# Performance work log

Hardware: AMD Instinct MI355X
Metric: run time of the kernel (lower is better)

Reference implementation:

```python
import jax, jax.numpy as jnp
import numpy as np

B, S, D = 2, 2048, 1024
H, KVH, HD = 16, 1, 64
E, K, HID = 8, 2, 4096
EPS = 1e-5


def rmsnorm(x, scale):
    ms = jnp.mean(x * x, axis=-1, keepdims=True)
    return x * jax.lax.rsqrt(ms + EPS) * scale


def setup_inputs() -> dict:
    key = jax.random.key(0)
    ks = jax.random.split(key, 12)
    s = lambda k, shape, fan: jax.random.normal(k, shape, jnp.float32) * (fan ** -0.5)
    return {
        "x": jax.random.normal(ks[0], (B, S, D), jnp.float32),
        "g_pre_mqa": jnp.ones((D,), jnp.float32),
        "g_post_mqa": jnp.ones((D,), jnp.float32),
        "g_pre_moe": jnp.ones((D,), jnp.float32),
        "g_post_moe": jnp.ones((D,), jnp.float32),
        "Wq": s(ks[1], (D, H * HD), D),
        "Wk": s(ks[2], (D, KVH * HD), D),
        "Wv": s(ks[3], (D, KVH * HD), D),
        "Wo": s(ks[4], (H * HD, D), H * HD),
        "Wg": s(ks[5], (D, E), D),
        "We1": s(ks[6], (E, D, HID), D),
        "We2": s(ks[7], (E, HID, D), HID),
    }


def mqa(x, Wq, Wk, Wv, Wo):
    b, s, _ = x.shape
    q = (x @ Wq).reshape(b, s, H, HD).transpose(0, 2, 1, 3)     # [B,H,S,hd]
    k = (x @ Wk).reshape(b, s, KVH, HD).transpose(0, 2, 1, 3)   # [B,1,S,hd]
    v = (x @ Wv).reshape(b, s, KVH, HD).transpose(0, 2, 1, 3)
    scores = jnp.einsum('bhqd,bhkd->bhqk', q, jnp.broadcast_to(k, (b, H, s, HD))) / np.sqrt(HD)
    probs = jax.nn.softmax(scores, axis=-1)  # note: no causal mask, matching _standard_attention
    out = jnp.einsum('bhqk,bhkd->bhqd', probs, jnp.broadcast_to(v, (b, H, s, HD)))
    out = out.transpose(0, 2, 1, 3).reshape(b, s, H * HD)
    return out @ Wo


def moe(h, Wg, We1, We2):
    logits = h @ Wg                       # [B,S,E]
    probs = jax.nn.softmax(logits, axis=-1)
    topv, topi = jax.lax.top_k(probs, K)  # [B,S,K]
    # scatter top-k probs into full expert vector (non-chosen experts -> 0)
    routing = jnp.sum(jax.nn.one_hot(topi, E, dtype=h.dtype) * topv[..., None], axis=-2)  # [B,S,E]
    mid = jax.nn.gelu(jnp.einsum('bsd,edh->bseh', h, We1))
    eo = jnp.einsum('bseh,ehd->bsed', mid, We2)
    out = jnp.einsum('bse,bsed->bsd', routing, eo)
    return out, probs


def reference(x, g_pre_mqa, g_post_mqa, g_pre_moe, g_post_moe, Wq, Wk, Wv, Wo, Wg, We1, We2):
    # inference path: dropout and router noise disabled (training=False)
    x = x + rmsnorm(mqa(rmsnorm(x, g_pre_mqa), Wq, Wk, Wv, Wo), g_post_mqa)
    moe_out, routing_probs = moe(rmsnorm(x, g_pre_moe), Wg, We1, We2)
    x = x + rmsnorm(moe_out, g_post_moe)
    return x, routing_probs
```

## Files before the change

kernel.cpp:

```cpp
#include <hip/hip_runtime.h>
#include <hip/hip_bf16.h>
#include <math.h>

#define NTOK   4096
#define DMODEL 1024
#define SEQL   2048
#define QKVW   1152
#define NH     16
#define HDIM   64
#define NE     8
#define HIDD   4096
#define EPSV   1e-5f
#define KT     32

#define ASCL   256.f
#define WSCL   4096.f
#define OUTSCL (1.f/1048576.f)
#define SSCALE (0.125f/65536.f)

typedef __attribute__((ext_vector_type(8))) short bf16x8;
typedef __attribute__((ext_vector_type(8))) _Float16 f16x8;
typedef __attribute__((ext_vector_type(4))) _Float16 f16x4;
typedef __attribute__((ext_vector_type(4))) float f32x4;

#define GLOBAL_AS __attribute__((address_space(1)))
#define LDS_AS    __attribute__((address_space(3)))
__device__ __forceinline__ void gl_lds16(const void* g, void* l){
  __builtin_amdgcn_global_load_lds((const GLOBAL_AS void*)g, (LDS_AS void*)l, 16u, 0, 0u);
}

__device__ __forceinline__ short f2b(float x){
  __hip_bfloat16 h = __float2bfloat16(x);
  return *reinterpret_cast<short*>(&h);
}
__device__ __forceinline__ float b2f(short s){
  __hip_bfloat16 h = *reinterpret_cast<__hip_bfloat16*>(&s);
  return __bfloat162float(h);
}
__device__ __forceinline__ void split3(float x, short& a, short& b, short& c){
  a = f2b(x);
  float r1 = x - b2f(a);
  b = f2b(r1);
  float r2 = r1 - b2f(b);
  c = f2b(r2);
}
__device__ __forceinline__ void split2h(float x, _Float16& a, _Float16& b){
  a = (_Float16)x;
  b = (_Float16)(x - (float)a);
}

__global__ __launch_bounds__(256) void transpose_conv_kernel(
    const float* __restrict__ in, short* __restrict__ out,
    int R, int C, long inb, long outb)
{
  __shared__ float tile[32][33];
  in  += (size_t)blockIdx.z * inb;
  out += (size_t)blockIdx.z * outb;
  int c0 = blockIdx.x*32, r0 = blockIdx.y*32;
  int tx = threadIdx.x & 31, ty = threadIdx.x >> 5;
  #pragma unroll
  for (int i=0;i<4;i++)
    tile[ty+i*8][tx] = in[(size_t)(r0+ty+i*8)*C + c0+tx];
  __syncthreads();
  #pragma unroll
  for (int i=0;i<4;i++)
    out[(size_t)(c0+ty+i*8)*R + r0+tx] = f2b(tile[tx][ty+i*8]);
}

__global__ __launch_bounds__(256) void transpose_split2f16_kernel(
    const float* __restrict__ in, _Float16* __restrict__ o1, _Float16* __restrict__ o2,
    int R, int C, int rowOff, int outLD)
{
  __shared__ float tile[32][33];
  int c0 = blockIdx.x*32, r0 = blockIdx.y*32;
  int tx = threadIdx.x & 31, ty = threadIdx.x >> 5;
  #pragma unroll
  for (int i=0;i<4;i++)
    tile[ty+i*8][tx] = in[(size_t)(r0+ty+i*8)*C + c0+tx];
  __syncthreads();
  #pragma unroll
  for (int i=0;i<4;i++){
    float v = tile[tx][ty+i*8] * WSCL;
    _Float16 a,b; split2h(v,a,b);
    size_t idx = (size_t)(c0+ty+i*8+rowOff)*outLD + r0+tx;
    o1[idx]=a; o2[idx]=b;
  }
}

__global__ __launch_bounds__(256) void rms_split2_kernel(
    const float* __restrict__ x, const float* __restrict__ g,
    _Float16* __restrict__ o1, _Float16* __restrict__ o2)
{
  int row = blockIdx.x, tid = threadIdx.x;
  const float4* xr = (const float4*)(x + (size_t)row*DMODEL);
  float4 v = xr[tid];
  float ss = v.x*v.x + v.y*v.y + v.z*v.z + v.w*v.w;
  #pragma unroll
  for (int off=32; off; off>>=1) ss += __shfl_down(ss, off);
  __shared__ float red[4];
  if ((tid&63)==0) red[tid>>6] = ss;
  __syncthreads();
  float rs = rsqrtf((red[0]+red[1]+red[2]+red[3])*(1.f/1024.f) + EPSV) * ASCL;
  float4 gv = ((const float4*)g)[tid];
  float o[4] = {v.x*rs*gv.x, v.y*rs*gv.y, v.z*rs*gv.z, v.w*rs*gv.w};
  f16x4 s1,s2;
  #pragma unroll
  for (int c=0;c<4;c++){ _Float16 a,b; split2h(o[c],a,b); s1[c]=a; s2[c]=b; }
  size_t base = (size_t)row*DMODEL + tid*4;
  *(f16x4*)(o1+base) = s1; *(f16x4*)(o2+base) = s2;
}

__global__ void split2_flat_kernel(const float* __restrict__ in,
    _Float16* __restrict__ o1, _Float16* __restrict__ o2, int n4)
{
  int i = blockIdx.x*256 + threadIdx.x;
  if (i >= n4) return;
  float4 v = ((const float4*)in)[i];
  float w[4] = {v.x*ASCL, v.y*ASCL, v.z*ASCL, v.w*ASCL};
  f16x4 s1,s2;
  #pragma unroll
  for (int c=0;c<4;c++){ _Float16 a,b; split2h(w[c],a,b); s1[c]=a; s2[c]=b; }
  ((f16x4*)o1)[i]=s1; ((f16x4*)o2)[i]=s2;
}

__global__ __launch_bounds__(256) void vtrans_split3_kernel(
    const float* __restrict__ qkv,
    short* __restrict__ o1, short* __restrict__ o2, short* __restrict__ o3)
{
  __shared__ float tile[32][33];
  int s0 = blockIdx.x*32, d0 = blockIdx.y*32, b = blockIdx.z;
  int tx = threadIdx.x & 31, ty = threadIdx.x >> 5;
  #pragma unroll
  for (int i=0;i<4;i++)
    tile[ty+i*8][tx] = qkv[(size_t)(b*SEQL + s0+ty+i*8)*QKVW + DMODEL+HDIM + d0+tx];
  __syncthreads();
  #pragma unroll
  for (int i=0;i<4;i++){
    float v = tile[tx][ty+i*8];
    short a,bs,c; split3(v,a,bs,c);
    size_t idx = (size_t)(b*HDIM + d0+ty+i*8)*SEQL + s0+tx;
    o1[idx]=a; o2[idx]=bs; o3[idx]=c;
  }
}

__global__ __launch_bounds__(256) void gemm_f16x2_kernel(
    const _Float16* __restrict__ a1, const _Float16* __restrict__ a2,
    const _Float16* __restrict__ b1, const _Float16* __restrict__ b2,
    float* __restrict__ C, int K, int ldc, float outscale)
{
  __shared__ _Float16 lsA[2][128*32];
  __shared__ _Float16 lsB[2][128*32];
  int m0 = blockIdx.y*128, n0 = blockIdx.x*128;
  int tid = threadIdx.x, wave = tid>>6, lane = tid&63;
  int g = lane>>4, li = lane&15;
  int wm = (wave>>1)*64, wn = (wave&1)*64;
  const _Float16* Ap[2] = {a1,a2};
  const _Float16* Bp[2] = {b1,b2};
  int srow = wave*32 + (lane>>2), scol = (lane&3)*8;
  const _Float16* gA[2][2]; const _Float16* gB[2][2];
  #pragma unroll
  for (int p=0;p<2;p++)
    #pragma unroll
    for (int i=0;i<2;i++){
      gA[p][i] = Ap[p] + (size_t)(m0+srow+i*16)*K + scol;
      gB[p][i] = Bp[p] + (size_t)(n0+srow+i*16)*K + scol;
    }
  f32x4 acc[4][4] = {};
  for (int k0=0; k0<K; k0+=32){
    #pragma unroll
    for (int p=0;p<2;p++)
      #pragma unroll
      for (int i=0;i<2;i++){
        gl_lds16(gA[p][i]+k0, &lsA[p][(wave*32+i*16)*32]);
        gl_lds16(gB[p][i]+k0, &lsB[p][(wave*32+i*16)*32]);
      }
    __syncthreads();
    #pragma unroll
    for (int i=0;i<2;i++){
      f16x8 af[4];
      #pragma unroll
      for (int m=0;m<4;m++) af[m] = *(f16x8*)&lsA[i][(wm+m*16+li)*32 + g*8];
      #pragma unroll
      for (int j=0;j<2-i;j++){
        #pragma unroll
        for (int n=0;n<4;n++){
          f16x8 bfr = *(f16x8*)&lsB[j][(wn+n*16+li)*32 + g*8];
          #pragma unroll
          for (int m=0;m<4;m++)
            acc[m][n] = __builtin_amdgcn_mfma_f32_16x16x32_f16(af[m], bfr, acc[m][n], 0,0,0);
        }
      }
    }
    __syncthreads();
  }
  #pragma unroll
  for (int m=0;m<4;m++){
    int lr0 = wm + m*16 + g*4;
    #pragma unroll
    for (int n=0;n<4;n++){
      int col = n0 + wn + n*16 + li;
      #pragma unroll
      for (int r=0;r<4;r++)
        C[(size_t)(m0+lr0+r)*ldc + col] = acc[m][n][r]*outscale;
    }
  }
}

__global__ __launch_bounds__(256) void attn_mix_kernel(
    const _Float16* __restrict__ q1, const _Float16* __restrict__ q2,
    const short* __restrict__ v1, const short* __restrict__ v2, const short* __restrict__ v3,
    _Float16* __restrict__ o1, _Float16* __restrict__ o2)
{
  __shared__ _Float16 Ks[32*136];
  __shared__ short Vs[64*104];
  int qt = blockIdx.x, h = blockIdx.y, b = blockIdx.z;
  int tid = threadIdx.x, wave = tid>>6, lane = tid&63;
  int g = lane>>4, li = lane&15;
  size_t qbase = (size_t)b*SEQL + qt*128;
  const _Float16* qsrc[2] = {q1,q2};
  const short* vsrc[3] = {v1,v2,v3};
  f16x8 qf[2][2][2];
  #pragma unroll
  for (int nf=0;nf<2;nf++){
    size_t qrow = qbase + wave*32 + nf*16 + li;
    #pragma unroll
    for (int j=0;j<2;j++)
      #pragma unroll
      for (int kk=0;kk<2;kk++)
        qf[nf][j][kk] = *(const f16x8*)(qsrc[j] + qrow*QKVW + h*HDIM + kk*32 + g*8);
  }
  float m_run[2] = {-1e30f,-1e30f}, l_run[2] = {0.f,0.f};
  f32x4 acc_o[4][2] = {};
  int src1 = (((2*g)&3)<<4) + li;
  int src2 = (((2*g+1)&3)<<4) + li;
  bool hi_half = (g>=2);

  for (int kvt=0; kvt<SEQL/KT; kvt++){
    __syncthreads();
    #pragma unroll
    for (int i=0;i<2;i++){
      int c = tid + 256*i;
      int row = c>>4, sub = c&15;
      int p = sub>>3, d = (sub&7)*8;
      *(f16x8*)&Ks[row*136 + p*64 + d] =
        *(const f16x8*)(qsrc[p] + ((size_t)b*SEQL + kvt*KT + row)*QKVW + DMODEL + d);
    }
    #pragma unroll
    for (int i=0;i<3;i++){
      int c = tid + 256*i;
      int row = c/12, sub = c - row*12;
      int p = sub>>2, s8 = (sub&3)*8;
      *(bf16x8*)&Vs[row*104 + p*32 + s8] =
        *(const bf16x8*)(vsrc[p] + ((size_t)b*HDIM + row)*SEQL + kvt*KT + s8);
    }
    __syncthreads();
    f32x4 s_acc[2][2] = {};
    #pragma unroll
    for (int i=0;i<2;i++){
      #pragma unroll
      for (int kk=0;kk<2;kk++){
        f16x8 af[2];
        #pragma unroll
        for (int mf=0;mf<2;mf++)
          af[mf] = *(f16x8*)&Ks[(mf*16+li)*136 + i*64 + kk*32 + g*8];
        #pragma unroll
        for (int j=0;j<2-i;j++){
          #pragma unroll
          for (int nf=0;nf<2;nf++){
            #pragma unroll
            for (int mf=0;mf<2;mf++)
              s_acc[mf][nf] = __builtin_amdgcn_mfma_f32_16x16x32_f16(af[mf], qf[nf][j][kk], s_acc[mf][nf], 0,0,0);
          }
        }
      }
    }
    float p[2][2][4];
    #pragma unroll
    for (int nf=0;nf<2;nf++){
      float mx = -1e30f;
      #pragma unroll
      for (int mf=0;mf<2;mf++)
        #pragma unroll
        for (int r=0;r<4;r++) mx = fmaxf(mx, s_acc[mf][nf][r]);
      mx = fmaxf(mx, __shfl_xor(mx,16));
      mx = fmaxf(mx, __shfl_xor(mx,32));
      mx *= SSCALE;
      if (!__all(mx <= m_run[nf] + 8.f)){
        float mn = fmaxf(m_run[nf], mx);
        float al = __expf(m_run[nf] - mn);
        m_run[nf] = mn;
        l_run[nf] *= al;
        #pragma unroll
        for (int mfd=0; mfd<4; mfd++){
          acc_o[mfd][nf][0]*=al; acc_o[mfd][nf][1]*=al;
          acc_o[mfd][nf][2]*=al; acc_o[mfd][nf][3]*=al;
        }
      }
      float rsum = 0.f;
      #pragma unroll
      for (int mf=0;mf<2;mf++)
        #pragma unroll
        for (int r=0;r<4;r++){
          float pv = __expf(s_acc[mf][nf][r]*SSCALE - m_run[nf]);
          p[mf][nf][r] = pv; rsum += pv;
        }
      rsum += __shfl_xor(rsum,16);
      rsum += __shfl_xor(rsum,32);
      l_run[nf] += rsum;
    }
    bf16x8 fp_frag[2][3];
    #pragma unroll
    for (int nf=0;nf<2;nf++){
      float p8[8];
      #pragma unroll
      for (int jj=0;jj<4;jj++){
        float v0 = __shfl(p[0][nf][jj], src1);
        float vv1 = __shfl(p[1][nf][jj], src1);
        p8[jj] = hi_half ? vv1 : v0;
        float w0 = __shfl(p[0][nf][jj], src2);
        float w1 = __shfl(p[1][nf][jj], src2);
        p8[4+jj] = hi_half ? w1 : w0;
      }
      #pragma unroll
      for (int jj=0;jj<8;jj++){
        short xa,xb,xc; split3(p8[jj], xa,xb,xc);
        fp_frag[nf][0][jj]=xa; fp_frag[nf][1][jj]=xb; fp_frag[nf][2][jj]=xc;
      }
    }
    #pragma unroll
    for (int vj=0;vj<3;vj++){
      bf16x8 av[4];
      #pragma unroll
      for (int mfd=0;mfd<4;mfd++)
        av[mfd] = *(bf16x8*)&Vs[(mfd*16+li)*104 + vj*32 + g*8];
      #pragma unroll
      for (int pi=0; pi<3-vj; pi++)
        #pragma unroll
        for (int mfd=0;mfd<4;mfd++)
          #pragma unroll
          for (int nf=0;nf<2;nf++)
            acc_o[mfd][nf] = __builtin_amdgcn_mfma_f32_16x16x32_bf16(av[mfd], fp_frag[nf][pi], acc_o[mfd][nf], 0,0,0);
    }
  }
  #pragma unroll
  for (int nf=0;nf<2;nf++){
    float inv = ASCL/l_run[nf];
    size_t q = qbase + wave*32 + nf*16 + li;
    #pragma unroll
    for (int mfd=0;mfd<4;mfd++){
      int d0 = mfd*16 + g*4;
      f16x4 sa,sb;
      #pragma unroll
      for (int r=0;r<4;r++){
        _Float16 xa,xb; split2h(acc_o[mfd][nf][r]*inv, xa,xb);
        sa[r]=xa; sb[r]=xb;
      }
      size_t base = q*DMODEL + h*HDIM + d0;
      *(f16x4*)(o1+base)=sa; *(f16x4*)(o2+base)=sb;
    }
  }
}

__global__ __launch_bounds__(256) void attnres_kernel(
    const float* __restrict__ x, const float* __restrict__ ao,
    const float* __restrict__ gpost, const float* __restrict__ gpre,
    float* __restrict__ x2, short* __restrict__ h)
{
  int row = blockIdx.x, tid = threadIdx.x;
  float4 a  = ((const float4*)(ao + (size_t)row*DMODEL))[tid];
  float4 xv = ((const float4*)(x  + (size_t)row*DMODEL))[tid];
  float ss = a.x*a.x + a.y*a.y + a.z*a.z + a.w*a.w;
  #pragma unroll
  for (int off=32; off; off>>=1) ss += __shfl_down(ss, off);
  __shared__ float red[4];
  if ((tid&63)==0) red[tid>>6] = ss;
  __syncthreads();
  float rs1 = rsqrtf((red[0]+red[1]+red[2]+red[3])*(1.f/1024.f) + EPSV);
  float4 gp = ((const float4*)gpost)[tid];
  float4 o;
  o.x = xv.x + a.x*rs1*gp.x; o.y = xv.y + a.y*rs1*gp.y;
  o.z = xv.z + a.z*rs1*gp.z; o.w = xv.w + a.w*rs1*gp.w;
  ((float4*)(x2 + (size_t)row*DMODEL))[tid] = o;
  float s2 = o.x*o.x + o.y*o.y + o.z*o.z + o.w*o.w;
  __syncthreads();
  #pragma unroll
  for (int off=32; off; off>>=1) s2 += __shfl_down(s2, off);
  if ((tid&63)==0) red[tid>>6] = s2;
  __syncthreads();
  float rs2 = rsqrtf((red[0]+red[1]+red[2]+red[3])*(1.f/1024.f) + EPSV);
  float4 gm = ((const float4*)gpre)[tid];
  short4 hs;
  hs.x = f2b(o.x*rs2*gm.x); hs.y = f2b(o.y*rs2*gm.y);
  hs.z = f2b(o.z*rs2*gm.z); hs.w = f2b(o.w*rs2*gm.w);
  *(short4*)(h + (size_t)row*DMODEL + tid*4) = hs;
}

__global__ __launch_bounds__(64) void router_kernel(
    const float* __restrict__ x2, const float* __restrict__ g, const float* __restrict__ Wg,
    float* __restrict__ probs_out, int* __restrict__ tok_list, float* __restrict__ w_list,
    int* __restrict__ counts)
{
  int t = blockIdx.x, lane = threadIdx.x;
  const float4* xr = (const float4*)(x2 + (size_t)t*DMODEL);
  float4 v[4]; float ss = 0.f;
  #pragma unroll
  for (int i=0;i<4;i++){ v[i] = xr[lane + 64*i];
    ss += v[i].x*v[i].x + v[i].y*v[i].y + v[i].z*v[i].z + v[i].w*v[i].w; }
  #pragma unroll
  for (int off=32; off; off>>=1) ss += __shfl_xor(ss, off);
  float rs = rsqrtf(ss*(1.f/1024.f) + EPSV);
  float le[8] = {0,0,0,0,0,0,0,0};
  #pragma unroll
  for (int i=0;i<4;i++){
    int jb = (lane + 64*i)*4;
    float hv[4] = {v[i].x, v[i].y, v[i].z, v[i].w};
    #pragma unroll
    for (int c=0;c<4;c++){
      float hj = hv[c]*rs*g[jb+c];
      const float* wrow = Wg + (size_t)(jb+c)*NE;
      #pragma unroll
      for (int ee=0;ee<8;ee++) le[ee] += hj*wrow[ee];
    }
  }
  #pragma unroll
  for (int ee=0;ee<8;ee++)
    #pragma unroll
    for (int off=32; off; off>>=1) le[ee] += __shfl_xor(le[ee], off);
  float mx = le[0];
  #pragma unroll
  for (int ee=1;ee<8;ee++) mx = fmaxf(mx, le[ee]);
  float p[8], s = 0.f;
  #pragma unroll
  for (int ee=0;ee<8;ee++){ p[ee] = expf(le[ee]-mx); s += p[ee]; }
  float inv = 1.f/s;
  #pragma unroll
  for (int ee=0;ee<8;ee++) p[ee] *= inv;
  if (lane < 8) probs_out[(size_t)t*NE + lane] = p[lane];
  if (lane == 0){
    int i1 = 0;
    #pragma unroll
    for (int ee=1;ee<8;ee++) if (p[ee] > p[i1]) i1 = ee;
    int i2 = (i1==0) ? 1 : 0;
    #pragma unroll
    for (int ee=0;ee<8;ee++) if (ee != i1 && p[ee] > p[i2]) i2 = ee;
    int pos = atomicAdd(&counts[i1], 1);
    tok_list[i1*NTOK+pos] = t;
    w_list[i1*NTOK+pos] = p[i1];
    pos = atomicAdd(&counts[i2], 1);
    tok_list[i2*NTOK+pos] = t | (1<<16);
    w_list[i2*NTOK+pos] = p[i2];
  }
}

__global__ void prefix_kernel(const int* __restrict__ counts, int* __restrict__ bases){
  if (threadIdx.x == 0){
    int a = 0;
    for (int ee=0;ee<8;ee++){ bases[ee] = a; a += counts[ee]; }
  }
}

__global__ __launch_bounds__(256) void moe_gemm1_kernel(
    const short* __restrict__ h, const short* __restrict__ we1t,
    const int* __restrict__ tok_list, const int* __restrict__ counts,
    const int* __restrict__ bases, short* __restrict__ mid)
{
  int e = blockIdx.z;
  int cnt = counts[e];
  int m0 = blockIdx.y*128, n0 = blockIdx.x*128;
  if (m0 >= cnt) return;
  int base = bases[e];
  const short* Bt = we1t + (size_t)e*HIDD*DMODEL;
  const int* tl = tok_list + e*NTOK;
  __shared__ short lsA[128*32];
  __shared__ short lsB[128*32];
  int tid = threadIdx.x, wave = tid>>6, lane = tid&63;
  int li = lane&15, g = lane>>4;
  int wm = (wave>>1)*64, wn = (wave&1)*64;
  int srow = wave*32 + (lane>>2), scol = (lane&3)*8;
  const short* gA[2]; const short* gB[2];
  #pragma unroll
  for (int i=0;i<2;i++){
    int rr = min(m0+srow+i*16, cnt-1);
    gA[i] = h + (size_t)(tl[rr] & 0xFFFF)*DMODEL + scol;
    gB[i] = Bt + (size_t)(n0+srow+i*16)*DMODEL + scol;
  }
  f32x4 acc[4][4] = {};
  for (int k0=0; k0<DMODEL; k0+=32){
    #pragma unroll
    for (int i=0;i<2;i++){
      gl_lds16(gA[i]+k0, &lsA[(wave*32+i*16)*32]);
      gl_lds16(gB[i]+k0, &lsB[(wave*32+i*16)*32]);
    }
    __syncthreads();
    bf16x8 af[4], bfr[4];
    #pragma unroll
    for (int m=0;m<4;m++) af[m] = *(bf16x8*)&lsA[(wm+m*16+li)*32 + g*8];
    #pragma unroll
    for (int n=0;n<4;n++) bfr[n] = *(bf16x8*)&lsB[(wn+n*16+li)*32 + g*8];
    #pragma unroll
    for (int m=0;m<4;m++)
      #pragma unroll
      for (int n=0;n<4;n++)
        acc[m][n] = __builtin_amdgcn_mfma_f32_16x16x32_bf16(af[m], bfr[n], acc[m][n], 0,0,0);
    __syncthreads();
  }
  #pragma unroll
  for (int m=0;m<4;m++){
    int lr0 = wm + m*16 + (g<<2);
    #pragma unroll
    for (int n=0;n<4;n++){
      int col = n0 + wn + n*16 + li;
      #pragma unroll
      for (int r=0;r<4;r++){
        int gr = m0 + lr0 + r;
        if (gr < cnt){
          float tval = acc[m][n][r];
          float u = 1.5957691216057308f*(tval + 0.044715f*tval*tval*tval);
          float ge = tval / (1.f + __expf(-u));
          mid[(size_t)(base+gr)*HIDD + col] = f2b(ge);
        }
      }
    }
  }
}

__global__ __launch_bounds__(256) void moe_gemm2_kernel(
    const short* __restrict__ mid, const short* __restrict__ we2t,
    const int* __restrict__ tok_list, const float* __restrict__ w_list,
    const int* __restrict__ counts, const int* __restrict__ bases,
    float* __restrict__ eo)
{
  int e = blockIdx.z;
  int cnt = counts[e];
  int m0 = blockIdx.y*128, n0 = blockIdx.x*128;
  if (m0 >= cnt) return;
  int base = bases[e];
  const short* A  = mid + (size_t)base*HIDD;
  const short* Bt = we2t + (size_t)e*DMODEL*HIDD;
  const int* tl = tok_list + e*NTOK;
  const float* wl = w_list + e*NTOK;
  __shared__ short lsA[128*32];
  __shared__ short lsB[128*32];
  int tid = threadIdx.x, wave = tid>>6, lane = tid&63;
  int li = lane&15, g = lane>>4;
  int wm = (wave>>1)*64, wn = (wave&1)*64;
  int srow = wave*32 + (lane>>2), scol = (lane&3)*8;
  const short* gA[2]; const short* gB[2];
  #pragma unroll
  for (int i=0;i<2;i++){
    int rr = min(m0+srow+i*16, cnt-1);
    gA[i] = A + (size_t)rr*HIDD + scol;
    gB[i] = Bt + (size_t)(n0+srow+i*16)*HIDD + scol;
  }
  f32x4 acc[4][4] = {};
  for (int k0=0; k0<HIDD; k0+=32){
    #pragma unroll
    for (int i=0;i<2;i++){
      gl_lds16(gA[i]+k0, &lsA[(wave*32+i*16)*32]);
      gl_lds16(gB[i]+k0, &lsB[(wave*32+i*16)*32]);
    }
    __syncthreads();
    bf16x8 af[4], bfr[4];
    #pragma unroll
    for (int m=0;m<4;m++) af[m] = *(bf16x8*)&lsA[(wm+m*16+li)*32 + g*8];
    #pragma unroll
    for (int n=0;n<4;n++) bfr[n] = *(bf16x8*)&lsB[(wn+n*16+li)*32 + g*8];
    #pragma unroll
    for (int m=0;m<4;m++)
      #pragma unroll
      for (int n=0;n<4;n++)
        acc[m][n] = __builtin_amdgcn_mfma_f32_16x16x32_bf16(af[m], bfr[n], acc[m][n], 0,0,0);
    __syncthreads();
  }
  #pragma unroll
  for (int m=0;m<4;m++){
    int lr0 = wm + m*16 + (g<<2);
    #pragma unroll
    for (int n=0;n<4;n++){
      int col = n0 + wn + n*16 + li;
      #pragma unroll
      for (int r=0;r<4;r++){
        int gr = m0 + lr0 + r;
        if (gr < cnt){
          int pv = tl[gr];
          eo[((size_t)(pv>>16)*NTOK + (pv & 0xFFFF))*DMODEL + col] = wl[gr]*acc[m][n][r];
        }
      }
    }
  }
}

__global__ __launch_bounds__(256) void final_kernel(
    const float* __restrict__ x2, const float* __restrict__ eo,
    const float* __restrict__ g, float* __restrict__ out)
{
  int row = blockIdx.x, tid = threadIdx.x;
  float4 m0 = ((const float4*)(eo + (size_t)row*DMODEL))[tid];
  float4 m1 = ((const float4*)(eo + (size_t)(NTOK+row)*DMODEL))[tid];
  float4 mv;
  mv.x = m0.x+m1.x; mv.y = m0.y+m1.y; mv.z = m0.z+m1.z; mv.w = m0.w+m1.w;
  float4 xv = ((const float4*)(x2  + (size_t)row*DMODEL))[tid];
  float ss = mv.x*mv.x + mv.y*mv.y + mv.z*mv.z + mv.w*mv.w;
  #pragma unroll
  for (int off=32; off; off>>=1) ss += __shfl_down(ss, off);
  __shared__ float red[4];
  if ((tid&63)==0) red[tid>>6] = ss;
  __syncthreads();
  float rs = rsqrtf((red[0]+red[1]+red[2]+red[3])*(1.f/1024.f) + EPSV);
  float4 gv = ((const float4*)g)[tid];
  float4 o;
  o.x = xv.x + mv.x*rs*gv.x; o.y = xv.y + mv.y*rs*gv.y;
  o.z = xv.z + mv.z*rs*gv.z; o.w = xv.w + mv.w*rs*gv.w;
  ((float4*)(out + (size_t)row*DMODEL))[tid] = o;
}

extern "C" void kernel_launch(void* const* d_in, const int* in_sizes, int n_in,
                              void* d_out, int out_size, void* d_ws, size_t ws_size,
                              hipStream_t stream) {
  (void)in_sizes; (void)n_in; (void)out_size; (void)ws_size;
  const float* x          = (const float*)d_in[0];
  const float* g_pre_mqa  = (const float*)d_in[1];
  const float* g_post_mqa = (const float*)d_in[2];
  const float* g_pre_moe  = (const float*)d_in[3];
  const float* g_post_moe = (const float*)d_in[4];
  const float* Wq         = (const float*)d_in[5];
  const float* Wk         = (const float*)d_in[6];
  const float* Wv         = (const float*)d_in[7];
  const float* Wo         = (const float*)d_in[8];
  const float* Wg         = (const float*)d_in[9];
  const float* We1        = (const float*)d_in[10];
  const float* We2        = (const float*)d_in[11];

  float* out_x = (float*)d_out;
  float* out_probs = out_x + (size_t)NTOK*DMODEL;

  char* p = (char*)d_ws;
  size_t off = 0;
  auto alloc = [&](size_t bytes)->char*{
    char* r = p + off; off = (off + bytes + 255) & ~(size_t)255; return r; };

  short* we1t = (short*)alloc((size_t)NE*HIDD*DMODEL*2);
  short* we2t = (short*)alloc((size_t)NE*DMODEL*HIDD*2);
  short* mid  = (short*)alloc((size_t)2*NTOK*HIDD*2);

  char* regA = alloc((size_t)2*NTOK*DMODEL*2);
  _Float16* xn1p1 = (_Float16*)regA;
  _Float16* xn1p2 = (_Float16*)(regA + (size_t)NTOK*DMODEL*2);
  float* ao       = (float*)regA;

  _Float16* wqkvT1 = (_Float16*)alloc((size_t)QKVW*DMODEL*2);
  _Float16* wqkvT2 = (_Float16*)alloc((size_t)QKVW*DMODEL*2);
  _Float16* woT1   = (_Float16*)alloc((size_t)DMODEL*DMODEL*2);
  _Float16* woT2   = (_Float16*)alloc((size_t)DMODEL*DMODEL*2);

  char* regB = alloc((size_t)NTOK*QKVW*4);
  float* qkv = (float*)regB;
  _Float16* attnp1 = (_Float16*)regB;
  _Float16* attnp2 = (_Float16*)(regB + (size_t)NTOK*DMODEL*2);

  char* regC = alloc((size_t)2*NTOK*DMODEL*4 + (size_t)NTOK*DMODEL*2);
  _Float16* qkvf1 = (_Float16*)regC;
  _Float16* qkvf2 = (_Float16*)(regC + (size_t)NTOK*QKVW*2);
  float* eo    = (float*)regC;
  short* hbuf  = (short*)(regC + (size_t)2*NTOK*DMODEL*4);

  short* vt1 = (short*)alloc((size_t)2*HDIM*SEQL*2);
  short* vt2 = (short*)alloc((size_t)2*HDIM*SEQL*2);
  short* vt3 = (short*)alloc((size_t)2*HDIM*SEQL*2);
  float* x2  = (float*)alloc((size_t)NTOK*DMODEL*4);
  int*   tok_l  = (int*)  alloc((size_t)NE*NTOK*4);
  float* w_l    = (float*)alloc((size_t)NE*NTOK*4);
  int*   counts = (int*)  alloc(256);
  int*   bases  = (int*)  alloc(256);

  transpose_conv_kernel<<<dim3(HIDD/32, DMODEL/32, NE), 256, 0, stream>>>(
      We1, we1t, DMODEL, HIDD, (long)DMODEL*HIDD, (long)HIDD*DMODEL);
  transpose_conv_kernel<<<dim3(DMODEL/32, HIDD/32, NE), 256, 0, stream>>>(
      We2, we2t, HIDD, DMODEL, (long)HIDD*DMODEL, (long)DMODEL*HIDD);
  transpose_split2f16_kernel<<<dim3(DMODEL/32, DMODEL/32), 256, 0, stream>>>(
      Wq, wqkvT1, wqkvT2, DMODEL, DMODEL, 0, DMODEL);
  transpose_split2f16_kernel<<<dim3(HDIM/32, DMODEL/32), 256, 0, stream>>>(
      Wk, wqkvT1, wqkvT2, DMODEL, HDIM, DMODEL, DMODEL);
  transpose_split2f16_kernel<<<dim3(HDIM/32, DMODEL/32), 256, 0, stream>>>(
      Wv, wqkvT1, wqkvT2, DMODEL, HDIM, DMODEL+HDIM, DMODEL);
  transpose_split2f16_kernel<<<dim3(DMODEL/32, DMODEL/32), 256, 0, stream>>>(
      Wo, woT1, woT2, DMODEL, DMODEL, 0, DMODEL);

  rms_split2_kernel<<<NTOK, 256, 0, stream>>>(x, g_pre_mqa, xn1p1, xn1p2);
  gemm_f16x2_kernel<<<dim3(QKVW/128, NTOK/128), 256, 0, stream>>>(
      xn1p1, xn1p2, wqkvT1, wqkvT2, qkv, DMODEL, QKVW, OUTSCL);
  split2_flat_kernel<<<(NTOK*QKVW/4 + 255)/256, 256, 0, stream>>>(
      qkv, qkvf1, qkvf2, NTOK*QKVW/4);
  vtrans_split3_kernel<<<dim3(SEQL/32, HDIM/32, 2), 256, 0, stream>>>(qkv, vt1, vt2, vt3);
  attn_mix_kernel<<<dim3(SEQL/128, NH, 2), 256, 0, stream>>>(
      qkvf1, qkvf2, vt1, vt2, vt3, attnp1, attnp2);
  gemm_f16x2_kernel<<<dim3(DMODEL/128, NTOK/128), 256, 0, stream>>>(
      attnp1, attnp2, woT1, woT2, ao, DMODEL, DMODEL, OUTSCL);
  attnres_kernel<<<NTOK, 256, 0, stream>>>(x, ao, g_post_mqa, g_pre_moe, x2, hbuf);

  hipMemsetAsync(counts, 0, 32, stream);
  router_kernel<<<NTOK, 64, 0, stream>>>(x2, g_pre_moe, Wg, out_probs, tok_l, w_l, counts);
  prefix_kernel<<<1, 64, 0, stream>>>(counts, bases);
  moe_gemm1_kernel<<<dim3(HIDD/128, NTOK/128, NE), 256, 0, stream>>>(
      hbuf, we1t, tok_l, counts, bases, mid);
  moe_gemm2_kernel<<<dim3(DMODEL/128, NTOK/128, NE), 256, 0, stream>>>(
      mid, we2t, tok_l, w_l, counts, bases, eo);
  final_kernel<<<NTOK, 256, 0, stream>>>(x2, eo, g_post_moe, out_x);
}
```

Baseline: 805.3 us.

## Switch attention PV product from bf16x3 split to f16x2 split

The PV stage of attention now splits probabilities and V into two fp16 pieces instead of three bf16 pieces. That cuts the MFMA count in the PV product from six to three per tile and shrinks the V staging in LDS. Probabilities are biased by a constant exponent offset (PBIAS) and V is prescaled so values stay in fp16 range, and the rescale threshold drops from 8 to 0.5 to keep exp values bounded. The MoE weight transpose also now writes 4-wide vectorised stores. The exchange is a narrower exponent range, which risks fp16 overflow or underflow and accuracy loss.

```diff
diff --git a/kernel.cpp b/kernel.cpp
--- a/kernel.cpp
+++ b/kernel.cpp
@@ -17,6 +17,8 @@
 #define WSCL   4096.f
 #define OUTSCL (1.f/1048576.f)
 #define SSCALE (0.125f/65536.f)
+#define PBIAS  10.397207708399179f
+#define DTHR   0.5f
 
 typedef __attribute__((ext_vector_type(8))) short bf16x8;
 typedef __attribute__((ext_vector_type(8))) _Float16 f16x8;
@@ -32,17 +34,6 @@
 __device__ __forceinline__ short f2b(float x){
   __hip_bfloat16 h = __float2bfloat16(x);
   return *reinterpret_cast<short*>(&h);
-}
-__device__ __forceinline__ float b2f(short s){
-  __hip_bfloat16 h = *reinterpret_cast<__hip_bfloat16*>(&s);
-  return __bfloat162float(h);
-}
-__device__ __forceinline__ void split3(float x, short& a, short& b, short& c){
-  a = f2b(x);
-  float r1 = x - b2f(a);
-  b = f2b(r1);
-  float r2 = r1 - b2f(b);
-  c = f2b(r2);
 }
 __device__ __forceinline__ void split2h(float x, _Float16& a, _Float16& b){
   a = (_Float16)x;
@@ -62,9 +53,13 @@
   for (int i=0;i<4;i++)
     tile[ty+i*8][tx] = in[(size_t)(r0+ty+i*8)*C + c0+tx];
   __syncthreads();
-  #pragma unroll
-  for (int i=0;i<4;i++)
-    out[(size_t)(c0+ty+i*8)*R + r0+tx] = f2b(tile[tx][ty+i*8]);
+  int cl = threadIdx.x >> 3, quad = threadIdx.x & 7;
+  short4 s;
+  s.x = f2b(tile[quad*4+0][cl]);
+  s.y = f2b(tile[quad*4+1][cl]);
+  s.z = f2b(tile[quad*4+2][cl]);
+  s.w = f2b(tile[quad*4+3][cl]);
+  *(short4*)&out[(size_t)(c0+cl)*R + r0 + quad*4] = s;
 }
 
 __global__ __launch_bounds__(256) void transpose_split2f16_kernel(
@@ -81,9 +76,9 @@
   #pragma unroll
   for (int i=0;i<4;i++){
     float v = tile[tx][ty+i*8] * WSCL;
-    _Float16 a,b; split2h(v,a,b);
+    _Float16 va,vb; split2h(v,va,vb);
     size_t idx = (size_t)(c0+ty+i*8+rowOff)*outLD + r0+tx;
-    o1[idx]=a; o2[idx]=b;
+    o1[idx]=va; o2[idx]=vb;
   }
 }
 
@@ -123,23 +118,23 @@
   ((f16x4*)o1)[i]=s1; ((f16x4*)o2)[i]=s2;
 }
 
-__global__ __launch_bounds__(256) void vtrans_split3_kernel(
+__global__ __launch_bounds__(256) void vtrans_split2_kernel(
     const float* __restrict__ qkv,
-    short* __restrict__ o1, short* __restrict__ o2, short* __restrict__ o3)
+    _Float16* __restrict__ o1, _Float16* __restrict__ o2)
 {
   __shared__ float tile[32][33];
-  int s0 = blockIdx.x*32, d0 = blockIdx.y*32, b = blockIdx.z;
+  int s0 = blockIdx.x*32, d0 = blockIdx.y*32, bb = blockIdx.z;
   int tx = threadIdx.x & 31, ty = threadIdx.x >> 5;
   #pragma unroll
   for (int i=0;i<4;i++)
-    tile[ty+i*8][tx] = qkv[(size_t)(b*SEQL + s0+ty+i*8)*QKVW + DMODEL+HDIM + d0+tx];
+    tile[ty+i*8][tx] = qkv[(size_t)(bb*SEQL + s0+ty+i*8)*QKVW + DMODEL+HDIM + d0+tx];
   __syncthreads();
   #pragma unroll
   for (int i=0;i<4;i++){
-    float v = tile[tx][ty+i*8];
-    short a,bs,c; split3(v,a,bs,c);
-    size_t idx = (size_t)(b*HDIM + d0+ty+i*8)*SEQL + s0+tx;
-    o1[idx]=a; o2[idx]=bs; o3[idx]=c;
+    float v = tile[tx][ty+i*8] * ASCL;
+    _Float16 va,vb; split2h(v,va,vb);
+    size_t idx = (size_t)(bb*HDIM + d0+ty+i*8)*SEQL + s0+tx;
+    o1[idx]=va; o2[idx]=vb;
   }
 }
 
@@ -206,19 +201,19 @@
   }
 }
 
-__global__ __launch_bounds__(256) void attn_mix_kernel(
+__global__ __launch_bounds__(256) void attn_f16_kernel(
     const _Float16* __restrict__ q1, const _Float16* __restrict__ q2,
-    const short* __restrict__ v1, const short* __restrict__ v2, const short* __restrict__ v3,
+    const _Float16* __restrict__ v1, const _Float16* __restrict__ v2,
     _Float16* __restrict__ o1, _Float16* __restrict__ o2)
 {
   __shared__ _Float16 Ks[32*136];
-  __shared__ short Vs[64*104];
+  __shared__ _Float16 Vs[64*72];
   int qt = blockIdx.x, h = blockIdx.y, b = blockIdx.z;
   int tid = threadIdx.x, wave = tid>>6, lane = tid&63;
   int g = lane>>4, li = lane&15;
   size_t qbase = (size_t)b*SEQL + qt*128;
   const _Float16* qsrc[2] = {q1,q2};
-  const short* vsrc[3] = {v1,v2,v3};
+  const _Float16* vsrc[2] = {v1,v2};
   f16x8 qf[2][2][2];
   #pragma unroll
   for (int nf=0;nf<2;nf++){
@@ -240,18 +235,18 @@
     #pragma unroll
     for (int i=0;i<2;i++){
       int c = tid + 256*i;
-      int row = c>>4, sub = c&15;
-      int p = sub>>3, d = (sub&7)*8;
-      *(f16x8*)&Ks[row*136 + p*64 + d] =
-        *(const f16x8*)(qsrc[p] + ((size_t)b*SEQL + kvt*KT + row)*QKVW + DMODEL + d);
-    }
-    #pragma unroll
-    for (int i=0;i<3;i++){
-      int c = tid + 256*i;
-      int row = c/12, sub = c - row*12;
-      int p = sub>>2, s8 = (sub&3)*8;
-      *(bf16x8*)&Vs[row*104 + p*32 + s8] =
-        *(const bf16x8*)(vsrc[p] + ((size_t)b*HDIM + row)*SEQL + kvt*KT + s8);
+      {
+        int row = c>>4, sub = c&15;
+        int pl = sub>>3, d = (sub&7)*8;
+        *(f16x8*)&Ks[row*136 + pl*64 + d] =
+          *(const f16x8*)(qsrc[pl] + ((size_t)b*SEQL + kvt*KT + row)*QKVW + DMODEL + d);
+      }
+      {
+        int row = c>>3, sub = c&7;
+        int pl = sub>>2, s8 = (sub&3)*8;
+        *(f16x8*)&Vs[row*72 + pl*32 + s8] =
+          *(const f16x8*)(vsrc[pl] + ((size_t)b*HDIM + row)*SEQL + kvt*KT + s8);
+      }
     }
     __syncthreads();
     f32x4 s_acc[2][2] = {};
@@ -285,7 +280,7 @@
       mx = fmaxf(mx, __shfl_xor(mx,16));
       mx = fmaxf(mx, __shfl_xor(mx,32));
       mx *= SSCALE;
-      if (!__all(mx <= m_run[nf] + 8.f)){
+      if (!__all(mx <= m_run[nf] + DTHR)){
         float mn = fmaxf(m_run[nf], mx);
         float al = __expf(m_run[nf] - mn);
         m_run[nf] = mn;
@@ -301,14 +296,14 @@
       for (int mf=0;mf<2;mf++)
         #pragma unroll
         for (int r=0;r<4;r++){
-          float pv = __expf(s_acc[mf][nf][r]*SSCALE - m_run[nf]);
+          float pv = __expf(s_acc[mf][nf][r]*SSCALE - m_run[nf] + PBIAS);
           p[mf][nf][r] = pv; rsum += pv;
         }
       rsum += __shfl_xor(rsum,16);
       rsum += __shfl_xor(rsum,32);
       l_run[nf] += rsum;
     }
-    bf16x8 fp_frag[2][3];
+    f16x8 fp_frag[2][2];
     #pragma unroll
     for (int nf=0;nf<2;nf++){
       float p8[8];
@@ -323,28 +318,28 @@
       }
       #pragma unroll
       for (int jj=0;jj<8;jj++){
-        short xa,xb,xc; split3(p8[jj], xa,xb,xc);
-        fp_frag[nf][0][jj]=xa; fp_frag[nf][1][jj]=xb; fp_frag[nf][2][jj]=xc;
-      }
-    }
-    #pragma unroll
-    for (int vj=0;vj<3;vj++){
-      bf16x8 av[4];
+        _Float16 xa,xb; split2h(p8[jj], xa,xb);
+        fp_frag[nf][0][jj]=xa; fp_frag[nf][1][jj]=xb;
+      }
+    }
+    #pragma unroll
+    for (int vj=0;vj<2;vj++){
+      f16x8 av[4];
       #pragma unroll
       for (int mfd=0;mfd<4;mfd++)
-        av[mfd] = *(bf16x8*)&Vs[(mfd*16+li)*104 + vj*32 + g*8];
-      #pragma unroll
-      for (int pi=0; pi<3-vj; pi++)
+        av[mfd] = *(f16x8*)&Vs[(mfd*16+li)*72 + vj*32 + g*8];
+      #pragma unroll
+      for (int pi=0; pi<2-vj; pi++)
         #pragma unroll
         for (int mfd=0;mfd<4;mfd++)
           #pragma unroll
           for (int nf=0;nf<2;nf++)
-            acc_o[mfd][nf] = __builtin_amdgcn_mfma_f32_16x16x32_bf16(av[mfd], fp_frag[nf][pi], acc_o[mfd][nf], 0,0,0);
+            acc_o[mfd][nf] = __builtin_amdgcn_mfma_f32_16x16x32_f16(av[mfd], fp_frag[nf][pi], acc_o[mfd][nf], 0,0,0);
     }
   }
   #pragma unroll
   for (int nf=0;nf<2;nf++){
-    float inv = ASCL/l_run[nf];
+    float inv = 1.f/l_run[nf];
     size_t q = qbase + wave*32 + nf*16 + li;
     #pragma unroll
     for (int mfd=0;mfd<4;mfd++){
@@ -664,9 +659,8 @@
   float* eo    = (float*)regC;
   short* hbuf  = (short*)(regC + (size_t)2*NTOK*DMODEL*4);
 
-  short* vt1 = (short*)alloc((size_t)2*HDIM*SEQL*2);
-  short* vt2 = (short*)alloc((size_t)2*HDIM*SEQL*2);
-  short* vt3 = (short*)alloc((size_t)2*HDIM*SEQL*2);
+  _Float16* vt1 = (_Float16*)alloc((size_t)2*HDIM*SEQL*2);
+  _Float16* vt2 = (_Float16*)alloc((size_t)2*HDIM*SEQL*2);
   float* x2  = (float*)alloc((size_t)NTOK*DMODEL*4);
   int*   tok_l  = (int*)  alloc((size_t)NE*NTOK*4);
   float* w_l    = (float*)alloc((size_t)NE*NTOK*4);
@@ -691,9 +685,9 @@
       xn1p1, xn1p2, wqkvT1, wqkvT2, qkv, DMODEL, QKVW, OUTSCL);
   split2_flat_kernel<<<(NTOK*QKVW/4 + 255)/256, 256, 0, stream>>>(
       qkv, qkvf1, qkvf2, NTOK*QKVW/4);
-  vtrans_split3_kernel<<<dim3(SEQL/32, HDIM/32, 2), 256, 0, stream>>>(qkv, vt1, vt2, vt3);
-  attn_mix_kernel<<<dim3(SEQL/128, NH, 2), 256, 0, stream>>>(
-      qkvf1, qkvf2, vt1, vt2, vt3, attnp1, attnp2);
+  vtrans_split2_kernel<<<dim3(SEQL/32, HDIM/32, 2), 256, 0, stream>>>(qkv, vt1, vt2);
+  attn_f16_kernel<<<dim3(SEQL/128, NH, 2), 256, 0, stream>>>(
+      qkvf1, qkvf2, vt1, vt2, attnp1, attnp2);
   gemm_f16x2_kernel<<<dim3(DMODEL/128, NTOK/128), 256, 0, stream>>>(
       attnp1, attnp2, woT1, woT2, ao, DMODEL, DMODEL, OUTSCL);
   attnres_kernel<<<NTOK, 256, 0, stream>>>(x, ao, g_post_mqa, g_pre_moe, x2, hbuf);
```

After: 771.9 us. -4.1%, faster.
